# Performance work log

Measured on AMD Instinct MI355X. Metric: run time of the kernel, lower is better.

Reference implementation:

```python
import jax, jax.numpy as jnp
import numpy as np

N, E, D_IN, H = 40000, 640000, 128, 128
R, B = 8, 30  # num_relations = 2*n_speakers**2, num_bases


def setup_inputs() -> dict:
    key = jax.random.key(0)
    ks = jax.random.split(key, 10)
    node_features = jax.random.normal(ks[0], (N, D_IN), jnp.float32)
    edge_index = jax.random.randint(ks[1], (2, E), 0, N)
    edge_type = jax.random.randint(ks[2], (E,), 0, R)
    edge_norm = jax.random.uniform(ks[3], (E,), jnp.float32)
    s_in = 1.0 / np.sqrt(D_IN)
    s_h = 1.0 / np.sqrt(H)
    basis = jax.random.normal(ks[4], (B, D_IN, H), jnp.float32) * s_in
    comp = jax.random.normal(ks[5], (R, B), jnp.float32) * (1.0 / np.sqrt(B))
    root = jax.random.normal(ks[6], (D_IN, H), jnp.float32) * s_in
    bias1 = jnp.zeros((H,), jnp.float32)
    w_rel = jax.random.normal(ks[7], (H, H), jnp.float32) * s_h
    w_root2 = jax.random.normal(ks[8], (H, H), jnp.float32) * s_h
    bias2 = jnp.zeros((H,), jnp.float32)
    return dict(node_features=node_features, edge_index=edge_index,
                edge_norm=edge_norm, edge_type=edge_type,
                basis=basis, comp=comp, root=root, bias1=bias1,
                w_rel=w_rel, w_root2=w_root2, bias2=bias2)


def reference(node_features, edge_index, edge_norm, edge_type,
              basis, comp, root, bias1, w_rel, w_root2, bias2):
    n = node_features.shape[0]
    src, dst = edge_index[0], edge_index[1]  # messages flow src -> dst

    # ---- RGCNConv (basis decomposition, mean aggregation, root + bias) ----
    # Per-relation weights from bases: [R, D_in, H]
    w = jnp.einsum('rb,bio->rio', comp, basis)
    # Transform all nodes by every relation once (avoids per-edge matmul): [R, N, H]
    xw = jnp.einsum('nd,rdo->rno', node_features, w)
    msgs = xw[edge_type, src]                                  # [E, H]
    agg = jax.ops.segment_sum(msgs, dst, num_segments=n)       # [N, H]
    deg = jax.ops.segment_sum(jnp.ones_like(dst, dtype=node_features.dtype),
                              dst, num_segments=n)
    agg = agg / jnp.maximum(deg, 1.0)[:, None]                 # mean aggregation
    h = agg + node_features @ root + bias1                     # [N, H]

    # ---- GraphConv (add aggregation): W_rel * sum_j x_j + W_root * x_i + b ----
    nbr = jax.ops.segment_sum(h[src], dst, num_segments=n)     # [N, H]
    out = nbr @ w_rel + h @ w_root2 + bias2
    return out
```

## Files before the change

### kernel.cpp

```cpp
#include <hip/hip_runtime.h>
#include <stdint.h>

#define DH 128
#define NB 30
#define NR 8

typedef short bf16x8 __attribute__((ext_vector_type(8)));
typedef float f32x4 __attribute__((ext_vector_type(4)));
typedef float f32x2 __attribute__((ext_vector_type(2)));

static __device__ __forceinline__ unsigned short f2bf(float f) {
    unsigned u = __float_as_uint(f);
    u += 0x7fffu + ((u >> 16) & 1u);
    return (unsigned short)(u >> 16);
}
static __device__ __forceinline__ float bflo(unsigned u) { return __uint_as_float(u << 16); }
static __device__ __forceinline__ float bfhi(unsigned u) { return __uint_as_float(u & 0xffff0000u); }

__global__ __launch_bounds__(256) void k_prephist(const float* __restrict__ comp,
                                                  const float* __restrict__ basis,
                                                  const float* __restrict__ root,
                                                  const float* __restrict__ wrel,
                                                  const float* __restrict__ wroot2,
                                                  unsigned short* __restrict__ wallT,
                                                  unsigned short* __restrict__ WT2,
                                                  const int* __restrict__ dstA, int E,
                                                  int* __restrict__ deg, int histB) {
    int b = blockIdx.x;
    int tid = threadIdx.x;
    if (b < histB) {
        int e = b * 256 + tid;
        if (e < E) atomicAdd(&deg[dstA[e]], 1);
        return;
    }
    int unit = (b - histB) * 2 + (tid >> 7);
    int o = tid & 127;
    int i = unit & 127;
    int y = unit >> 7;
    if (y < NR) {
        float s = 0.f;
        #pragma unroll
        for (int bb = 0; bb < NB; ++bb)
            s += comp[y * NB + bb] * basis[((size_t)bb * DH + i) * DH + o];
        wallT[((size_t)y * DH + o) * DH + i] = f2bf(s);
    } else if (y == NR) {
        wallT[((size_t)NR * DH + o) * DH + i] = f2bf(root[i * DH + o]);
    } else {
        const float* W = (y == NR + 2) ? wroot2 : wrel;
        WT2[((size_t)(y - NR - 1) * DH + o) * DH + i] = f2bf(W[i * DH + o]);
    }
}

__global__ __launch_bounds__(1024) void k_scan(const int* __restrict__ deg, int n, int total_n,
                                               int* __restrict__ offsets,
                                               int* __restrict__ cursor,
                                               unsigned long long* __restrict__ st,
                                               int* __restrict__ ticket) {
    __shared__ int s[1024];
    __shared__ int bid_s, pre_s;
    const int tid = threadIdx.x;
    if (tid == 0) bid_s = atomicAdd(ticket, 1);
    __syncthreads();
    const int b = bid_s;
    int i = b * 1024 + tid;
    int v = (i < n) ? deg[i] : 0;
    s[tid] = v;
    __syncthreads();
    for (int off = 1; off < 1024; off <<= 1) {
        int t = (tid >= off) ? s[tid - off] : 0;
        __syncthreads();
        s[tid] += t;
        __syncthreads();
    }
    if (tid == 0) {
        int total = s[1023];
        atomicExch(&st[b], (1ULL << 62) | (unsigned long long)(unsigned)total);
        long long pre = 0;
        int t = b - 1;
        while (t >= 0) {
            unsigned long long w;
            do { w = atomicAdd(&st[t], 0ULL); } while (w == 0ULL);
            pre += (long long)(w & 0x3FFFFFFFFFFFFFFFULL);
            if ((w >> 62) == 2ULL) break;
            --t;
        }
        atomicExch(&st[b], (2ULL << 62) | (unsigned long long)(pre + total));
        pre_s = (int)pre;
    }
    __syncthreads();
    int ov = pre_s + s[tid] - v;
    if (i < total_n) offsets[i] = ov;
    if (i < n) cursor[i] = ov;
}

__global__ __launch_bounds__(256) void k_gemm1s(const float* __restrict__ x,
                                                const unsigned short* __restrict__ wallT,
                                                const float* __restrict__ bias1,
                                                int Nn,
                                                unsigned* __restrict__ xw8,
                                                unsigned short* __restrict__ hb,
                                                const int* __restrict__ src,
                                                const int* __restrict__ dstA,
                                                const int* __restrict__ etype, int E,
                                                int* __restrict__ cursor,
                                                unsigned* __restrict__ sorted,
                                                int gemmB, int gx) {
    __shared__ __align__(16) unsigned short As[128][136];
    __shared__ __align__(16) unsigned short Bs[128][136];
    const int tid = threadIdx.x;
    const int b = blockIdx.x;

    if (b >= gemmB) {
        const int stride = (gridDim.x - gemmB) * 256;
        for (int e = (b - gemmB) * 256 + tid; e < E; e += stride) {
            int d = dstA[e];
            int pos = atomicAdd(&cursor[d], 1);
            sorted[pos] = (unsigned)src[e] | ((unsigned)etype[e] << 17);
        }
        return;
    }

    const int wave = tid >> 6, lane = tid & 63;
    const int g = b / gx;
    const int rowbase = (b % gx) * 128;
    const int lq = lane >> 4, lr = lane & 15;

    #pragma unroll
    for (int it = 0; it < 8; ++it) {
        int c = it * 256 + tid;
        int row = c >> 4, col = c & 15;
        int rg = rowbase + row; if (rg >= Nn) rg = Nn - 1;
        float4 v0 = *(const float4*)&x[(size_t)rg * DH + col * 8];
        float4 v1 = *(const float4*)&x[(size_t)rg * DH + col * 8 + 4];
        uint4 u;
        u.x = (unsigned)f2bf(v0.x) | ((unsigned)f2bf(v0.y) << 16);
        u.y = (unsigned)f2bf(v0.z) | ((unsigned)f2bf(v0.w) << 16);
        u.z = (unsigned)f2bf(v1.x) | ((unsigned)f2bf(v1.y) << 16);
        u.w = (unsigned)f2bf(v1.z) | ((unsigned)f2bf(v1.w) << 16);
        *(uint4*)&As[row][col * 8] = u;
    }

    for (int rr = 0; rr < 3; ++rr) {
        const int r = g * 3 + rr;
        const unsigned short* WT = wallT + (size_t)r * DH * DH;
        if (rr) __syncthreads();
        #pragma unroll
        for (int it = 0; it < 8; ++it) {
            int c = it * 256 + tid;
            int row = c >> 4, col = c & 15;
            *(uint4*)&Bs[row][col * 8] = *(const uint4*)&WT[(size_t)row * DH + col * 8];
        }
        __syncthreads();

        f32x4 acc[2][8];
        #pragma unroll
        for (int mt = 0; mt < 2; ++mt)
            #pragma unroll
            for (int nt = 0; nt < 8; ++nt) acc[mt][nt] = (f32x4)0.f;

        #pragma unroll
        for (int ks = 0; ks < 4; ++ks) {
            const int ko = ks * 32 + lq * 8;
            bf16x8 a0 = *(const bf16x8*)&As[wave * 32 + lr][ko];
            bf16x8 a1 = *(const bf16x8*)&As[wave * 32 + 16 + lr][ko];
            #pragma unroll
            for (int nt = 0; nt < 8; ++nt) {
                bf16x8 bb = *(const bf16x8*)&Bs[nt * 16 + lr][ko];
                acc[0][nt] = __builtin_amdgcn_mfma_f32_16x16x32_bf16(a0, bb, acc[0][nt], 0, 0, 0);
                acc[1][nt] = __builtin_amdgcn_mfma_f32_16x16x32_bf16(a1, bb, acc[1][nt], 0, 0, 0);
            }
        }
        __syncthreads();

        float bv[8];
        #pragma unroll
        for (int nt = 0; nt < 8; ++nt) bv[nt] = (r == NR) ? bias1[nt * 16 + lr] : 0.f;
        #pragma unroll
        for (int mt = 0; mt < 2; ++mt)
            #pragma unroll
            for (int nt = 0; nt < 8; ++nt)
                #pragma unroll
                for (int reg = 0; reg < 4; ++reg) {
                    int ml = wave * 32 + mt * 16 + lq * 4 + reg;
                    Bs[ml][nt * 16 + lr] = f2bf(acc[mt][nt][reg] + bv[nt]);
                }
        __syncthreads();

        if (r < NR) {
            unsigned* dst = xw8 + ((size_t)r * Nn + rowbase) * (DH / 4);
            #pragma unroll
            for (int it = 0; it < 8; ++it) {
                int c = it * 256 + tid;
                int row = c >> 4, col = c & 15;
                if (rowbase + row < Nn) {
                    uint4 q = *(uint4*)&Bs[row][col * 8];
                    uint2 o;
                    o.x = __builtin_amdgcn_cvt_pk_fp8_f32(bflo(q.x), bfhi(q.x), 0, false);
                    o.x = __builtin_amdgcn_cvt_pk_fp8_f32(bflo(q.y), bfhi(q.y), o.x, true);
                    o.y = __builtin_amdgcn_cvt_pk_fp8_f32(bflo(q.z), bfhi(q.z), 0, false);
                    o.y = __builtin_amdgcn_cvt_pk_fp8_f32(bflo(q.w), bfhi(q.w), o.y, true);
                    *(uint2*)&dst[(size_t)row * (DH / 4) + col * 2] = o;
                }
            }
        } else {
            #pragma unroll
            for (int it = 0; it < 8; ++it) {
                int c = it * 256 + tid;
                int row = c >> 4, col = c & 15;
                if (rowbase + row < Nn)
                    *(uint4*)&hb[((size_t)(rowbase + row)) * DH + col * 8] = *(uint4*)&Bs[row][col * 8];
            }
        }
    }
}

__global__ __launch_bounds__(256) void k_agg1(const int* __restrict__ offsets,
                                              const unsigned* __restrict__ sorted,
                                              const unsigned* __restrict__ xw8,
                                              const unsigned* __restrict__ hb32,
                                              int Nn, unsigned* __restrict__ hbf) {
    int w = (blockIdx.x * blockDim.x + threadIdx.x) >> 6;
    if (w >= Nn) return;
    int lane = threadIdx.x & 63;
    int half = lane >> 5, sub = lane & 31;
    int s = offsets[w], e = offsets[w + 1];
    float a0 = 0.f, a1 = 0.f, a2 = 0.f, a3 = 0.f;
    int p = s;
    for (; p + 16 <= e; p += 16) {
        unsigned pk[8];
        #pragma unroll
        for (int j = 0; j < 8; ++j) pk[j] = sorted[p + 2 * j + half];
        unsigned u[8];
        #pragma unroll
        for (int j = 0; j < 8; ++j)
            u[j] = xw8[((size_t)(pk[j] >> 17) * Nn + (pk[j] & 0x1FFFFu)) * 32 + sub];
        #pragma unroll
        for (int j = 0; j < 8; ++j) {
            f32x2 lo = __builtin_amdgcn_cvt_pk_f32_fp8(u[j], false);
            f32x2 hi = __builtin_amdgcn_cvt_pk_f32_fp8(u[j], true);
            a0 += lo.x; a1 += lo.y; a2 += hi.x; a3 += hi.y;
        }
    }
    if (p < e) {
        unsigned pk[8]; float m[8];
        #pragma unroll
        for (int j = 0; j < 8; ++j) {
            int q = p + 2 * j + half; bool v = q < e;
            pk[j] = sorted[v ? q : e - 1];
            m[j] = v ? 1.f : 0.f;
        }
        unsigned u[8];
        #pragma unroll
        for (int j = 0; j < 8; ++j)
            u[j] = xw8[((size_t)(pk[j] >> 17) * Nn + (pk[j] & 0x1FFFFu)) * 32 + sub];
        #pragma unroll
        for (int j = 0; j < 8; ++j) {
            f32x2 lo = __builtin_amdgcn_cvt_pk_f32_fp8(u[j], false);
            f32x2 hi = __builtin_amdgcn_cvt_pk_f32_fp8(u[j], true);
            a0 = fmaf(m[j], lo.x, a0);
            a1 = fmaf(m[j], lo.y, a1);
            a2 = fmaf(m[j], hi.x, a2);
            a3 = fmaf(m[j], hi.y, a3);
        }
    }
    a0 += __shfl_xor(a0, 32, 64);
    a1 += __shfl_xor(a1, 32, 64);
    a2 += __shfl_xor(a2, 32, 64);
    a3 += __shfl_xor(a3, 32, 64);
    if (half == 0) {
        float invd = 1.0f / fmaxf((float)(e - s), 1.0f);
        uint2 hv = *(const uint2*)&hb32[(size_t)w * 64 + sub * 2];
        float h0 = bflo(hv.x) + a0 * invd;
        float h1 = bfhi(hv.x) + a1 * invd;
        float h2 = bflo(hv.y) + a2 * invd;
        float h3 = bfhi(hv.y) + a3 * invd;
        uint2 o;
        o.x = (unsigned)f2bf(h0) | ((unsigned)f2bf(h1) << 16);
        o.y = (unsigned)f2bf(h2) | ((unsigned)f2bf(h3) << 16);
        *(uint2*)&hbf[(size_t)w * 64 + sub * 2] = o;
    }
}

__global__ __launch_bounds__(256) void k_agg2(const int* __restrict__ offsets,
                                              const unsigned* __restrict__ sorted,
                                              const uint2* __restrict__ hbf2,
                                              int Nn, uint2* __restrict__ nbr2) {
    int w = (blockIdx.x * blockDim.x + threadIdx.x) >> 6;
    if (w >= Nn) return;
    int lane = threadIdx.x & 63;
    int half = lane >> 5, sub = lane & 31;
    int s = offsets[w], e = offsets[w + 1];
    float a0 = 0.f, a1 = 0.f, a2 = 0.f, a3 = 0.f;
    int p = s;
    for (; p + 16 <= e; p += 16) {
        unsigned pk[8];
        #pragma unroll
        for (int j = 0; j < 8; ++j) pk[j] = sorted[p + 2 * j + half];
        uint2 u[8];
        #pragma unroll
        for (int j = 0; j < 8; ++j)
            u[j] = hbf2[(size_t)(pk[j] & 0x1FFFFu) * 32 + sub];
        #pragma unroll
        for (int j = 0; j < 8; ++j) {
            a0 += bflo(u[j].x); a1 += bfhi(u[j].x);
            a2 += bflo(u[j].y); a3 += bfhi(u[j].y);
        }
    }
    if (p < e) {
        unsigned pk[8]; float m[8];
        #pragma unroll
        for (int j = 0; j < 8; ++j) {
            int q = p + 2 * j + half; bool v = q < e;
            pk[j] = sorted[v ? q : e - 1];
            m[j] = v ? 1.f : 0.f;
        }
        uint2 u[8];
        #pragma unroll
        for (int j = 0; j < 8; ++j)
            u[j] = hbf2[(size_t)(pk[j] & 0x1FFFFu) * 32 + sub];
        #pragma unroll
        for (int j = 0; j < 8; ++j) {
            a0 = fmaf(m[j], bflo(u[j].x), a0);
            a1 = fmaf(m[j], bfhi(u[j].x), a1);
            a2 = fmaf(m[j], bflo(u[j].y), a2);
            a3 = fmaf(m[j], bfhi(u[j].y), a3);
        }
    }
    a0 += __shfl_xor(a0, 32, 64);
    a1 += __shfl_xor(a1, 32, 64);
    a2 += __shfl_xor(a2, 32, 64);
    a3 += __shfl_xor(a3, 32, 64);
    if (half == 0) {
        uint2 o;
        o.x = (unsigned)f2bf(a0) | ((unsigned)f2bf(a1) << 16);
        o.y = (unsigned)f2bf(a2) | ((unsigned)f2bf(a3) << 16);
        nbr2[(size_t)w * 32 + sub] = o;
    }
}

__global__ __launch_bounds__(256) void k_gemm2m(const unsigned short* __restrict__ nbrbf,
                                                const unsigned short* __restrict__ hbf,
                                                const unsigned short* __restrict__ WT2,
                                                const float* __restrict__ bias2,
                                                int Nn, float* __restrict__ out) {
    __shared__ __align__(16) unsigned short As[128][136];
    __shared__ __align__(16) unsigned short Bs[128][136];
    const int tid = threadIdx.x;
    const int wave = tid >> 6, lane = tid & 63;
    const int rowbase = blockIdx.x * 128;
    const int lq = lane >> 4, lr = lane & 15;

    f32x4 acc[2][8];
    #pragma unroll
    for (int mt = 0; mt < 2; ++mt)
        #pragma unroll
        for (int nt = 0; nt < 8; ++nt) acc[mt][nt] = (f32x4)0.f;

    for (int ph = 0; ph < 2; ++ph) {
        const unsigned short* A = ph ? hbf : nbrbf;
        const unsigned short* WT = WT2 + (size_t)ph * DH * DH;
        if (ph) __syncthreads();
        #pragma unroll
        for (int it = 0; it < 8; ++it) {
            int c = it * 256 + tid;
            int row = c >> 4, col = c & 15;
            int rg = rowbase + row; if (rg >= Nn) rg = Nn - 1;
            *(uint4*)&As[row][col * 8] = *(const uint4*)&A[(size_t)rg * DH + col * 8];
            *(uint4*)&Bs[row][col * 8] = *(const uint4*)&WT[(size_t)row * DH + col * 8];
        }
        __syncthreads();
        #pragma unroll
        for (int ks = 0; ks < 4; ++ks) {
            const int ko = ks * 32 + lq * 8;
            bf16x8 a0 = *(const bf16x8*)&As[wave * 32 + lr][ko];
            bf16x8 a1 = *(const bf16x8*)&As[wave * 32 + 16 + lr][ko];
            #pragma unroll
            for (int nt = 0; nt < 8; ++nt) {
                bf16x8 b = *(const bf16x8*)&Bs[nt * 16 + lr][ko];
                acc[0][nt] = __builtin_amdgcn_mfma_f32_16x16x32_bf16(a0, b, acc[0][nt], 0, 0, 0);
                acc[1][nt] = __builtin_amdgcn_mfma_f32_16x16x32_bf16(a1, b, acc[1][nt], 0, 0, 0);
            }
        }
    }

    float bv[8];
    #pragma unroll
    for (int nt = 0; nt < 8; ++nt) bv[nt] = bias2[nt * 16 + lr];
    #pragma unroll
    for (int mt = 0; mt < 2; ++mt)
        #pragma unroll
        for (int nt = 0; nt < 8; ++nt)
            #pragma unroll
            for (int reg = 0; reg < 4; ++reg) {
                int m = rowbase + wave * 32 + mt * 16 + lq * 4 + reg;
                if (m < Nn) out[(size_t)m * DH + nt * 16 + lr] = acc[mt][nt][reg] + bv[nt];
            }
}

extern "C" void kernel_launch(void* const* d_in, const int* in_sizes, int n_in,
                              void* d_out, int out_size, void* d_ws, size_t ws_size,
                              hipStream_t stream) {
    const float* x      = (const float*)d_in[0];
    const int*   eidx   = (const int*)d_in[1];
    const int*   etype  = (const int*)d_in[3];
    const float* basis  = (const float*)d_in[4];
    const float* comp   = (const float*)d_in[5];
    const float* root   = (const float*)d_in[6];
    const float* bias1  = (const float*)d_in[7];
    const float* wrel   = (const float*)d_in[8];
    const float* wroot2 = (const float*)d_in[9];
    const float* bias2  = (const float*)d_in[10];
    float* out = (float*)d_out;

    const int N = in_sizes[0] / DH;
    const int E = in_sizes[3];
    const int* srcA = eidx;
    const int* dstA = eidx + E;

    char* ws = (char*)d_ws;
    size_t off = 0;
    auto alloc = [&](size_t bytes) -> void* {
        void* p = (void*)(ws + off);
        off += (bytes + 255) & ~(size_t)255;
        return p;
    };
    int* deg           = (int*)alloc((size_t)N * 4);
    unsigned long long* st = (unsigned long long*)alloc(64 * 8);
    int* ticket        = (int*)alloc(256);
    int* cursor        = (int*)alloc((size_t)N * 4);
    int* offsets       = (int*)alloc((size_t)(N + 1) * 4);
    unsigned* sorted   = (unsigned*)alloc((size_t)E * 4);
    unsigned short* wallT = (unsigned short*)alloc((size_t)(NR + 1) * DH * DH * 2);
    unsigned short* WT2   = (unsigned short*)alloc((size_t)2 * DH * DH * 2);
    unsigned* xw8      = (unsigned*)alloc((size_t)NR * N * DH);
    unsigned short* hb = (unsigned short*)alloc((size_t)N * DH * 2);
    unsigned* hbf      = (unsigned*)alloc((size_t)N * (DH / 2) * 4);
    unsigned* nbrbf    = (unsigned*)alloc((size_t)N * (DH / 2) * 4);
    (void)ws_size; (void)n_in; (void)out_size;

    hipMemsetAsync(deg, 0, (size_t)N * 4 + 768, stream);

    const int histB = (E + 255) / 256;
    k_prephist<<<histB + 704, 256, 0, stream>>>(comp, basis, root, wrel, wroot2,
                                                wallT, WT2, dstA, E, deg, histB);

    const int totn = N + 1;
    const int nsb = (totn + 1023) / 1024;
    k_scan<<<nsb, 1024, 0, stream>>>(deg, N, totn, offsets, cursor, st, ticket);

    const int gx = (N + 127) / 128;
    const int gemmB = gx * 3;
    const int scatB = 1280;
    k_gemm1s<<<gemmB + scatB, 256, 0, stream>>>(x, wallT, bias1, N, xw8, hb,
                                                srcA, dstA, etype, E, cursor, sorted,
                                                gemmB, gx);

    k_agg1<<<(N * 64) / 256, 256, 0, stream>>>(offsets, sorted, xw8,
                                               (const unsigned*)hb, N, hbf);
    k_agg2<<<(N * 64) / 256, 256, 0, stream>>>(offsets, sorted, (const uint2*)hbf, N, (uint2*)nbrbf);
    k_gemm2m<<<gx, 256, 0, stream>>>((const unsigned short*)nbrbf, (const unsigned short*)hbf,
                                     WT2, bias2, N, out);
}
```

Measured before the change: 240.2 us.

## Keep GEMM A-tile in registers, drop As shared buffer, scatter blocks first

The fused GEMM/scatter kernel now loads each wave's rows of x straight into bf16 MFMA operand registers, so the As shared-memory tile and its LDS reads are gone. Shared memory per block is roughly halved, and launch_bounds(256,4) asks for four resident blocks per CU. The block order is also flipped so the edge-scatter blocks launch first and the GEMM blocks after them. The risk is higher register pressure from holding the A fragments, plus global loads of x that are less coalesced.

```diff
diff --git a/kernel.cpp b/kernel.cpp
--- a/kernel.cpp
+++ b/kernel.cpp
@@ -93,26 +93,25 @@
     if (i < n) cursor[i] = ov;
 }
 
-__global__ __launch_bounds__(256) void k_gemm1s(const float* __restrict__ x,
-                                                const unsigned short* __restrict__ wallT,
-                                                const float* __restrict__ bias1,
-                                                int Nn,
-                                                unsigned* __restrict__ xw8,
-                                                unsigned short* __restrict__ hb,
-                                                const int* __restrict__ src,
-                                                const int* __restrict__ dstA,
-                                                const int* __restrict__ etype, int E,
-                                                int* __restrict__ cursor,
-                                                unsigned* __restrict__ sorted,
-                                                int gemmB, int gx) {
-    __shared__ __align__(16) unsigned short As[128][136];
+__global__ __launch_bounds__(256, 4) void k_gemm1s(const float* __restrict__ x,
+                                                   const unsigned short* __restrict__ wallT,
+                                                   const float* __restrict__ bias1,
+                                                   int Nn,
+                                                   unsigned* __restrict__ xw8,
+                                                   unsigned short* __restrict__ hb,
+                                                   const int* __restrict__ src,
+                                                   const int* __restrict__ dstA,
+                                                   const int* __restrict__ etype, int E,
+                                                   int* __restrict__ cursor,
+                                                   unsigned* __restrict__ sorted,
+                                                   int scatB, int gx) {
     __shared__ __align__(16) unsigned short Bs[128][136];
     const int tid = threadIdx.x;
     const int b = blockIdx.x;
 
-    if (b >= gemmB) {
-        const int stride = (gridDim.x - gemmB) * 256;
-        for (int e = (b - gemmB) * 256 + tid; e < E; e += stride) {
+    if (b < scatB) {
+        const int stride = scatB * 256;
+        for (int e = b * 256 + tid; e < E; e += stride) {
             int d = dstA[e];
             int pos = atomicAdd(&cursor[d], 1);
             sorted[pos] = (unsigned)src[e] | ((unsigned)etype[e] << 17);
@@ -120,24 +119,29 @@
         return;
     }
 
+    const int bg = b - scatB;
     const int wave = tid >> 6, lane = tid & 63;
-    const int g = b / gx;
-    const int rowbase = (b % gx) * 128;
+    const int g = bg / gx;
+    const int rowbase = (bg % gx) * 128;
     const int lq = lane >> 4, lr = lane & 15;
 
+    bf16x8 a[2][4];
     #pragma unroll
-    for (int it = 0; it < 8; ++it) {
-        int c = it * 256 + tid;
-        int row = c >> 4, col = c & 15;
-        int rg = rowbase + row; if (rg >= Nn) rg = Nn - 1;
-        float4 v0 = *(const float4*)&x[(size_t)rg * DH + col * 8];
-        float4 v1 = *(const float4*)&x[(size_t)rg * DH + col * 8 + 4];
-        uint4 u;
-        u.x = (unsigned)f2bf(v0.x) | ((unsigned)f2bf(v0.y) << 16);
-        u.y = (unsigned)f2bf(v0.z) | ((unsigned)f2bf(v0.w) << 16);
-        u.z = (unsigned)f2bf(v1.x) | ((unsigned)f2bf(v1.y) << 16);
-        u.w = (unsigned)f2bf(v1.z) | ((unsigned)f2bf(v1.w) << 16);
-        *(uint4*)&As[row][col * 8] = u;
+    for (int mt = 0; mt < 2; ++mt) {
+        int rg = rowbase + wave * 32 + mt * 16 + lr;
+        if (rg >= Nn) rg = Nn - 1;
+        const float* xr = &x[(size_t)rg * DH];
+        #pragma unroll
+        for (int ks = 0; ks < 4; ++ks) {
+            float4 v0 = *(const float4*)&xr[ks * 32 + lq * 8];
+            float4 v1 = *(const float4*)&xr[ks * 32 + lq * 8 + 4];
+            bf16x8 pk;
+            pk[0] = (short)f2bf(v0.x); pk[1] = (short)f2bf(v0.y);
+            pk[2] = (short)f2bf(v0.z); pk[3] = (short)f2bf(v0.w);
+            pk[4] = (short)f2bf(v1.x); pk[5] = (short)f2bf(v1.y);
+            pk[6] = (short)f2bf(v1.z); pk[7] = (short)f2bf(v1.w);
+            a[mt][ks] = pk;
+        }
     }
 
     for (int rr = 0; rr < 3; ++rr) {
@@ -161,13 +165,11 @@
         #pragma unroll
         for (int ks = 0; ks < 4; ++ks) {
             const int ko = ks * 32 + lq * 8;
-            bf16x8 a0 = *(const bf16x8*)&As[wave * 32 + lr][ko];
-            bf16x8 a1 = *(const bf16x8*)&As[wave * 32 + 16 + lr][ko];
             #pragma unroll
             for (int nt = 0; nt < 8; ++nt) {
                 bf16x8 bb = *(const bf16x8*)&Bs[nt * 16 + lr][ko];
-                acc[0][nt] = __builtin_amdgcn_mfma_f32_16x16x32_bf16(a0, bb, acc[0][nt], 0, 0, 0);
-                acc[1][nt] = __builtin_amdgcn_mfma_f32_16x16x32_bf16(a1, bb, acc[1][nt], 0, 0, 0);
+                acc[0][nt] = __builtin_amdgcn_mfma_f32_16x16x32_bf16(a[0][ks], bb, acc[0][nt], 0, 0, 0);
+                acc[1][nt] = __builtin_amdgcn_mfma_f32_16x16x32_bf16(a[1][ks], bb, acc[1][nt], 0, 0, 0);
             }
         }
         __syncthreads();
@@ -451,9 +453,9 @@
     const int gx = (N + 127) / 128;
     const int gemmB = gx * 3;
     const int scatB = 1280;
-    k_gemm1s<<<gemmB + scatB, 256, 0, stream>>>(x, wallT, bias1, N, xw8, hb,
+    k_gemm1s<<<scatB + gemmB, 256, 0, stream>>>(x, wallT, bias1, N, xw8, hb,
                                                 srcA, dstA, etype, E, cursor, sorted,
-                                                gemmB, gx);
+                                                scatB, gx);
 
     k_agg1<<<(N * 64) / 256, 256, 0, stream>>>(offsets, sorted, xw8,
                                                (const unsigned*)hb, N, hbf);
```

Measured after the change: 291.0 us. 21.2% more time.

## Halve gemm1 row tile to 64 and schedule scatter blocks first

Applied to the files above, without the earlier changes.

Reduces the fused gemm+scatter kernel's row tile from 128 to 64, cutting LDS and accumulator registers so three blocks fit per CU, and doubles the gemm block count. Scatter blocks are moved to the front of the grid so the atomic edge sort starts early and overlaps with gemm work. The trade is that each weight tile is reloaded into LDS for half as many rows, raising weight-load traffic per output. The second gemm's grid is recomputed to keep its 128-row tiling.

```diff
diff --git a/kernel.cpp b/kernel.cpp
--- a/kernel.cpp
+++ b/kernel.cpp
@@ -93,26 +93,26 @@
     if (i < n) cursor[i] = ov;
 }
 
-__global__ __launch_bounds__(256) void k_gemm1s(const float* __restrict__ x,
-                                                const unsigned short* __restrict__ wallT,
-                                                const float* __restrict__ bias1,
-                                                int Nn,
-                                                unsigned* __restrict__ xw8,
-                                                unsigned short* __restrict__ hb,
-                                                const int* __restrict__ src,
-                                                const int* __restrict__ dstA,
-                                                const int* __restrict__ etype, int E,
-                                                int* __restrict__ cursor,
-                                                unsigned* __restrict__ sorted,
-                                                int gemmB, int gx) {
-    __shared__ __align__(16) unsigned short As[128][136];
+__global__ __launch_bounds__(256, 3) void k_gemm1s(const float* __restrict__ x,
+                                                   const unsigned short* __restrict__ wallT,
+                                                   const float* __restrict__ bias1,
+                                                   int Nn,
+                                                   unsigned* __restrict__ xw8,
+                                                   unsigned short* __restrict__ hb,
+                                                   const int* __restrict__ src,
+                                                   const int* __restrict__ dstA,
+                                                   const int* __restrict__ etype, int E,
+                                                   int* __restrict__ cursor,
+                                                   unsigned* __restrict__ sorted,
+                                                   int scatB, int gx) {
+    __shared__ __align__(16) unsigned short As[64][136];
     __shared__ __align__(16) unsigned short Bs[128][136];
     const int tid = threadIdx.x;
     const int b = blockIdx.x;
 
-    if (b >= gemmB) {
-        const int stride = (gridDim.x - gemmB) * 256;
-        for (int e = (b - gemmB) * 256 + tid; e < E; e += stride) {
+    if (b < scatB) {
+        const int stride = scatB * 256;
+        for (int e = b * 256 + tid; e < E; e += stride) {
             int d = dstA[e];
             int pos = atomicAdd(&cursor[d], 1);
             sorted[pos] = (unsigned)src[e] | ((unsigned)etype[e] << 17);
@@ -120,13 +120,14 @@
         return;
     }
 
+    const int bg = b - scatB;
     const int wave = tid >> 6, lane = tid & 63;
-    const int g = b / gx;
-    const int rowbase = (b % gx) * 128;
+    const int g = bg / gx;
+    const int rowbase = (bg % gx) * 64;
     const int lq = lane >> 4, lr = lane & 15;
 
     #pragma unroll
-    for (int it = 0; it < 8; ++it) {
+    for (int it = 0; it < 4; ++it) {
         int c = it * 256 + tid;
         int row = c >> 4, col = c & 15;
         int rg = rowbase + row; if (rg >= Nn) rg = Nn - 1;
@@ -152,22 +153,18 @@
         }
         __syncthreads();
 
-        f32x4 acc[2][8];
-        #pragma unroll
-        for (int mt = 0; mt < 2; ++mt)
-            #pragma unroll
-            for (int nt = 0; nt < 8; ++nt) acc[mt][nt] = (f32x4)0.f;
+        f32x4 acc[8];
+        #pragma unroll
+        for (int nt = 0; nt < 8; ++nt) acc[nt] = (f32x4)0.f;
 
         #pragma unroll
         for (int ks = 0; ks < 4; ++ks) {
             const int ko = ks * 32 + lq * 8;
-            bf16x8 a0 = *(const bf16x8*)&As[wave * 32 + lr][ko];
-            bf16x8 a1 = *(const bf16x8*)&As[wave * 32 + 16 + lr][ko];
+            bf16x8 a0 = *(const bf16x8*)&As[wave * 16 + lr][ko];
             #pragma unroll
             for (int nt = 0; nt < 8; ++nt) {
                 bf16x8 bb = *(const bf16x8*)&Bs[nt * 16 + lr][ko];
-                acc[0][nt] = __builtin_amdgcn_mfma_f32_16x16x32_bf16(a0, bb, acc[0][nt], 0, 0, 0);
-                acc[1][nt] = __builtin_amdgcn_mfma_f32_16x16x32_bf16(a1, bb, acc[1][nt], 0, 0, 0);
+                acc[nt] = __builtin_amdgcn_mfma_f32_16x16x32_bf16(a0, bb, acc[nt], 0, 0, 0);
             }
         }
         __syncthreads();
@@ -176,20 +173,18 @@
         #pragma unroll
         for (int nt = 0; nt < 8; ++nt) bv[nt] = (r == NR) ? bias1[nt * 16 + lr] : 0.f;
         #pragma unroll
-        for (int mt = 0; mt < 2; ++mt)
-            #pragma unroll
-            for (int nt = 0; nt < 8; ++nt)
-                #pragma unroll
-                for (int reg = 0; reg < 4; ++reg) {
-                    int ml = wave * 32 + mt * 16 + lq * 4 + reg;
-                    Bs[ml][nt * 16 + lr] = f2bf(acc[mt][nt][reg] + bv[nt]);
-                }
+        for (int nt = 0; nt < 8; ++nt)
+            #pragma unroll
+            for (int reg = 0; reg < 4; ++reg) {
+                int ml = wave * 16 + lq * 4 + reg;
+                Bs[ml][nt * 16 + lr] = f2bf(acc[nt][reg] + bv[nt]);
+            }
         __syncthreads();
 
         if (r < NR) {
             unsigned* dst = xw8 + ((size_t)r * Nn + rowbase) * (DH / 4);
             #pragma unroll
-            for (int it = 0; it < 8; ++it) {
+            for (int it = 0; it < 4; ++it) {
                 int c = it * 256 + tid;
                 int row = c >> 4, col = c & 15;
                 if (rowbase + row < Nn) {
@@ -204,7 +199,7 @@
             }
         } else {
             #pragma unroll
-            for (int it = 0; it < 8; ++it) {
+            for (int it = 0; it < 4; ++it) {
                 int c = it * 256 + tid;
                 int row = c >> 4, col = c & 15;
                 if (rowbase + row < Nn)
@@ -448,16 +443,16 @@
     const int nsb = (totn + 1023) / 1024;
     k_scan<<<nsb, 1024, 0, stream>>>(deg, N, totn, offsets, cursor, st, ticket);
 
-    const int gx = (N + 127) / 128;
+    const int gx = (N + 63) / 64;
     const int gemmB = gx * 3;
     const int scatB = 1280;
-    k_gemm1s<<<gemmB + scatB, 256, 0, stream>>>(x, wallT, bias1, N, xw8, hb,
+    k_gemm1s<<<scatB + gemmB, 256, 0, stream>>>(x, wallT, bias1, N, xw8, hb,
                                                 srcA, dstA, etype, E, cursor, sorted,
-                                                gemmB, gx);
+                                                scatB, gx);
 
     k_agg1<<<(N * 64) / 256, 256, 0, stream>>>(offsets, sorted, xw8,
                                                (const unsigned*)hb, N, hbf);
     k_agg2<<<(N * 64) / 256, 256, 0, stream>>>(offsets, sorted, (const uint2*)hbf, N, (uint2*)nbrbf);
-    k_gemm2m<<<gx, 256, 0, stream>>>((const unsigned short*)nbrbf, (const unsigned short*)hbf,
+    k_gemm2m<<<gx / 2 + (N % 128 ? 1 : 0), 256, 0, stream>>>((const unsigned short*)nbrbf, (const unsigned short*)hbf,
                                      WT2, bias2, N, out);
 }
```

Result: no change. 238.4 us (-0.7%).
